# Kernel optimization log

Measured on AMD Instinct MI355X. Metric: run time of the kernel, lower is better.

The kernel has to match this reference:

```python
import jax, jax.numpy as jnp
import numpy as np

N_TOKENS = 262144
D_IN = 128
D_OUT = 128
N_EXPERTS = 8


def setup_inputs() -> dict:
    key = jax.random.key(0)
    k1, k2, k3, k4 = jax.random.split(key, 4)
    x = jax.random.normal(k1, (N_TOKENS, D_IN), dtype=jnp.float32)
    split = jax.random.randint(k2, (N_TOKENS,), 0, N_EXPERTS, dtype=jnp.int64)
    # Per-expert Linear params (one "model" per unique split value).
    W = jax.random.normal(k3, (N_EXPERTS, D_IN, D_OUT), dtype=jnp.float32) / np.sqrt(D_IN)
    b = jax.random.normal(k4, (N_EXPERTS, D_OUT), dtype=jnp.float32)
    return {"x": x, "split": split, "W": W, "b": b}


def reference(x, split, W, b):
    # Original 'alone' path: gather rows per unique split value, apply
    # model[split_value], concat, then reorder via argsort of the gathered
    # indices. That composition is exactly a per-token expert apply:
    #   out[t] = x[t] @ W[split[t]] + b[split[t]]
    # Computed densely per expert (fixed shapes, jit-friendly), then select.
    y_all = jnp.einsum('nf,efg->eng', x, W) + b[:, None, :]  # [E, N, d_out]
    tok = jnp.arange(x.shape[0])
    return y_all[split, tok]  # [N, d_out]
```

## Files before the change

kernel.cpp:

```cpp
#include <hip/hip_runtime.h>


typedef __bf16 bf16x8 __attribute__((ext_vector_type(8)));
typedef unsigned short u16x8 __attribute__((ext_vector_type(8)));
typedef float f32x4 __attribute__((ext_vector_type(4)));

__device__ __forceinline__ unsigned short f2bf(float f) {
    unsigned u = __builtin_bit_cast(unsigned, f);
    u += 0x7FFFu + ((u >> 16) & 1u);
    return (unsigned short)(u >> 16);
}
__device__ __forceinline__ unsigned pack2(float a, float b) {
    return (unsigned)f2bf(a) | ((unsigned)f2bf(b) << 16);
}

__global__ void k_wt(const float* __restrict__ W, unsigned short* __restrict__ Wt) {
    __shared__ float T[16][132];
    int e = blockIdx.x >> 3;
    int g0 = (blockIdx.x & 7) << 4;
    const float* We = W + e * 128 * 128;
    #pragma unroll
    for (int i = 0; i < 2; ++i) {
        int idx = i * 256 + threadIdx.x;
        int f = idx >> 2, q = idx & 3;
        float4 v = *(const float4*)(We + f * 128 + g0 + q * 4);
        T[q * 4 + 0][f] = v.x; T[q * 4 + 1][f] = v.y;
        T[q * 4 + 2][f] = v.z; T[q * 4 + 3][f] = v.w;
    }
    __syncthreads();
    int g = threadIdx.x >> 4, fc = threadIdx.x & 15;
    u16x8 o;
    #pragma unroll
    for (int j = 0; j < 8; ++j) o[j] = f2bf(T[g][fc * 8 + j]);
    *(u16x8*)(Wt + ((e * 128 + g0 + g) * 128 + fc * 8)) = o;
}

#define NT 256

__global__ __launch_bounds__(512) void k_fused(
    const float* __restrict__ x, const int* __restrict__ split,
    const float* __restrict__ bias, const unsigned short* __restrict__ Wt,
    float* __restrict__ out) {

    __shared__ unsigned short A[NT * 128];
    __shared__ int hcnt[8], startE[8];
    __shared__ int dest[NT], trow[NT];
    __shared__ int exT[24], rbT[24], limT[24];
    __shared__ int Tn;

    const int tid = threadIdx.x;
    const long t0 = (long)blockIdx.x * NT;

    if (tid < 8) hcnt[tid] = 0;
    __syncthreads();

    float4 xv[16];
    const float* xb = x + t0 * 128;
    #pragma unroll
    for (int rr = 0; rr < 16; ++rr)
        xv[rr] = *(const float4*)(xb + (rr * 512 + tid) * 4);

    int e = 0, rank = 0;
    if (tid < NT) {
        e = split[t0 + tid];
        rank = atomicAdd(&hcnt[e], 1);
    }
    __syncthreads();

    if (tid == 0) {
        int acc = 0, T = 0;
        for (int ee = 0; ee < 8; ++ee) {
            int c = hcnt[ee];
            startE[ee] = acc;
            for (int k = 0; k < c; k += 16) {
                exT[T] = ee; rbT[T] = acc + k;
                limT[T] = (c - k < 16) ? (c - k) : 16; T++;
            }
            acc += c;
        }
        Tn = T;
    }
    __syncthreads();

    if (tid < NT) {
        int s = startE[e] + rank;
        dest[tid] = s;
        trow[s] = tid;
    }
    __syncthreads();

    #pragma unroll
    for (int rr = 0; rr < 16; ++rr) {
        int c = rr * 512 + tid;
        int row = c >> 5;
        int s = dest[row];
        int fc = (c & 31) >> 1;
        int half = c & 1;
        unsigned d0 = pack2(xv[rr].x, xv[rr].y);
        unsigned d1 = pack2(xv[rr].z, xv[rr].w);
        unsigned short* p = A + s * 128 + ((fc ^ (s & 7)) << 3) + half * 4;
        *(uint2*)p = make_uint2(d0, d1);
    }
    __syncthreads();

    const int lane = tid & 63, w = tid >> 6;
    const int l15 = lane & 15, lq = lane >> 4;
    const int T = Tn;

    bf16x8 bfrag[4];
    float bv = 0.f;
    int preve = -1;

    for (int tau = 0; tau < T; ++tau) {
        int ee = exT[tau], rb = rbT[tau], lim = limT[tau];
        if (ee != preve) {
            preve = ee;
            const unsigned short* Wb = Wt + ee * 16384 + (w * 16 + l15) * 128;
            #pragma unroll
            for (int kk = 0; kk < 4; ++kk)
                bfrag[kk] = *(const bf16x8*)(Wb + (kk * 4 + lq) * 8);
            bv = bias[ee * 128 + w * 16 + l15];
        }
        int srow = rb + l15;
        srow = srow < NT - 1 ? srow : NT - 1;
        f32x4 acc = {0.f, 0.f, 0.f, 0.f};
        #pragma unroll
        for (int kk = 0; kk < 4; ++kk) {
            int fc = kk * 4 + lq;
            bf16x8 a = *(const bf16x8*)(A + srow * 128 + ((fc ^ (srow & 7)) << 3));
            acc = __builtin_amdgcn_mfma_f32_16x16x32_bf16(a, bfrag[kk], acc, 0, 0, 0);
        }
        #pragma unroll
        for (int r = 0; r < 4; ++r) {
            int ri = lq * 4 + r;
            if (ri < lim) {
                int tokl = trow[rb + ri];
                out[(t0 + tokl) * 128 + w * 16 + l15] = acc[r] + bv;
            }
        }
    }
}

extern "C" void kernel_launch(void* const* d_in, const int* in_sizes, int n_in,
                              void* d_out, int out_size, void* d_ws, size_t ws_size,
                              hipStream_t stream) {
    const float* x     = (const float*)d_in[0];
    const int*   split = (const int*)d_in[1];
    const float* W     = (const float*)d_in[2];
    const float* bias  = (const float*)d_in[3];
    float* out = (float*)d_out;

    int n = in_sizes[1];
    unsigned short* Wt = (unsigned short*)d_ws;

    k_wt<<<64, 256, 0, stream>>>(W, Wt);
    k_fused<<<n / NT, 512, 0, stream>>>(x, split, bias, Wt, out);
}
```

Measured before the change: 83.02 us.

## Halve block tokens, use 4 waves with two output tiles each, ballot-based expert ranking

```diff
diff --git a/kernel.cpp b/kernel.cpp
--- a/kernel.cpp
+++ b/kernel.cpp
@@ -35,55 +35,64 @@
     *(u16x8*)(Wt + ((e * 128 + g0 + g) * 128 + fc * 8)) = o;
 }
 
-#define NT 256
+#define NT 128
 
-__global__ __launch_bounds__(512) void k_fused(
+__global__ __launch_bounds__(256, 4) void k_fused(
     const float* __restrict__ x, const int* __restrict__ split,
     const float* __restrict__ bias, const unsigned short* __restrict__ Wt,
     float* __restrict__ out) {
 
     __shared__ unsigned short A[NT * 128];
-    __shared__ int hcnt[8], startE[8];
+    __shared__ int wcnt[16];
+    __shared__ int startE[8], off1[8];
     __shared__ int dest[NT], trow[NT];
-    __shared__ int exT[24], rbT[24], limT[24];
+    __shared__ int exT[16], rbT[16], limT[16];
     __shared__ int Tn;
 
     const int tid = threadIdx.x;
+    const int lane = tid & 63, w = tid >> 6;
     const long t0 = (long)blockIdx.x * NT;
-
-    if (tid < 8) hcnt[tid] = 0;
-    __syncthreads();
 
     float4 xv[16];
     const float* xb = x + t0 * 128;
     #pragma unroll
     for (int rr = 0; rr < 16; ++rr)
-        xv[rr] = *(const float4*)(xb + (rr * 512 + tid) * 4);
+        xv[rr] = *(const float4*)(xb + (rr * 256 + tid) * 4);
 
-    int e = 0, rank = 0;
-    if (tid < NT) {
-        e = split[t0 + tid];
-        rank = atomicAdd(&hcnt[e], 1);
+    int e = 255, myrank = 0;
+    if (tid < NT) e = split[t0 + tid];
+    const unsigned long long below = (lane == 63) ? ~0ull >> 1 : (1ull << lane) - 1;
+    #pragma unroll
+    for (int ee = 0; ee < 8; ++ee) {
+        unsigned long long m = __ballot(e == ee);
+        if (e == ee) myrank = (int)__popcll(m & below);
+        if (w < 2 && lane == ee) wcnt[w * 8 + ee] = (int)__popcll(m);
     }
     __syncthreads();
 
-    if (tid == 0) {
-        int acc = 0, T = 0;
-        for (int ee = 0; ee < 8; ++ee) {
-            int c = hcnt[ee];
-            startE[ee] = acc;
-            for (int k = 0; k < c; k += 16) {
-                exT[T] = ee; rbT[T] = acc + k;
-                limT[T] = (c - k < 16) ? (c - k) : 16; T++;
-            }
-            acc += c;
+    if (w == 0 && lane < 8) {
+        int c0 = wcnt[lane], c1 = wcnt[8 + lane];
+        int cE = c0 + c1;
+        int v = cE;
+        #pragma unroll
+        for (int d = 1; d < 8; d <<= 1) { int t2 = __shfl_up(v, d, 64); if (lane >= d) v += t2; }
+        int sE = v - cE;
+        startE[lane] = sE; off1[lane] = sE + c0;
+        int nt = (cE + 15) >> 4;
+        int u = nt;
+        #pragma unroll
+        for (int d = 1; d < 8; d <<= 1) { int t2 = __shfl_up(u, d, 64); if (lane >= d) u += t2; }
+        int tb = u - nt;
+        for (int k = 0; k < nt; ++k) {
+            exT[tb + k] = lane; rbT[tb + k] = sE + k * 16;
+            int rem = cE - k * 16; limT[tb + k] = rem < 16 ? rem : 16;
         }
-        Tn = T;
+        if (lane == 7) Tn = u;
     }
     __syncthreads();
 
     if (tid < NT) {
-        int s = startE[e] + rank;
+        int s = (w == 0 ? startE[e] : off1[e]) + myrank;
         dest[tid] = s;
         trow[s] = tid;
     }
@@ -91,51 +100,54 @@
 
     #pragma unroll
     for (int rr = 0; rr < 16; ++rr) {
-        int c = rr * 512 + tid;
+        int c = rr * 256 + tid;
         int row = c >> 5;
         int s = dest[row];
         int fc = (c & 31) >> 1;
         int half = c & 1;
         unsigned d0 = pack2(xv[rr].x, xv[rr].y);
         unsigned d1 = pack2(xv[rr].z, xv[rr].w);
-        unsigned short* p = A + s * 128 + ((fc ^ (s & 7)) << 3) + half * 4;
-        *(uint2*)p = make_uint2(d0, d1);
+        *(uint2*)(A + s * 128 + ((fc ^ (s & 7)) << 3) + half * 4) = make_uint2(d0, d1);
     }
     __syncthreads();
 
-    const int lane = tid & 63, w = tid >> 6;
     const int l15 = lane & 15, lq = lane >> 4;
     const int T = Tn;
 
-    bf16x8 bfrag[4];
-    float bv = 0.f;
+    bf16x8 bfrag[2][4];
+    float bv[2];
     int preve = -1;
 
     for (int tau = 0; tau < T; ++tau) {
         int ee = exT[tau], rb = rbT[tau], lim = limT[tau];
         if (ee != preve) {
             preve = ee;
-            const unsigned short* Wb = Wt + ee * 16384 + (w * 16 + l15) * 128;
             #pragma unroll
-            for (int kk = 0; kk < 4; ++kk)
-                bfrag[kk] = *(const bf16x8*)(Wb + (kk * 4 + lq) * 8);
-            bv = bias[ee * 128 + w * 16 + l15];
+            for (int j = 0; j < 2; ++j) {
+                const unsigned short* Wb = Wt + ee * 16384 + (w * 32 + j * 16 + l15) * 128;
+                #pragma unroll
+                for (int kk = 0; kk < 4; ++kk)
+                    bfrag[j][kk] = *(const bf16x8*)(Wb + (kk * 4 + lq) * 8);
+                bv[j] = bias[ee * 128 + w * 32 + j * 16 + l15];
+            }
         }
         int srow = rb + l15;
-        srow = srow < NT - 1 ? srow : NT - 1;
-        f32x4 acc = {0.f, 0.f, 0.f, 0.f};
+        srow = srow < NT ? srow : NT - 1;
+        f32x4 acc0 = {0.f, 0.f, 0.f, 0.f}, acc1 = {0.f, 0.f, 0.f, 0.f};
         #pragma unroll
         for (int kk = 0; kk < 4; ++kk) {
             int fc = kk * 4 + lq;
             bf16x8 a = *(const bf16x8*)(A + srow * 128 + ((fc ^ (srow & 7)) << 3));
-            acc = __builtin_amdgcn_mfma_f32_16x16x32_bf16(a, bfrag[kk], acc, 0, 0, 0);
+            acc0 = __builtin_amdgcn_mfma_f32_16x16x32_bf16(a, bfrag[0][kk], acc0, 0, 0, 0);
+            acc1 = __builtin_amdgcn_mfma_f32_16x16x32_bf16(a, bfrag[1][kk], acc1, 0, 0, 0);
         }
         #pragma unroll
         for (int r = 0; r < 4; ++r) {
             int ri = lq * 4 + r;
             if (ri < lim) {
-                int tokl = trow[rb + ri];
-                out[(t0 + tokl) * 128 + w * 16 + l15] = acc[r] + bv;
+                long o = (t0 + trow[rb + ri]) * 128 + w * 32 + l15;
+                out[o]      = acc0[r] + bv[0];
+                out[o + 16] = acc1[r] + bv[1];
             }
         }
     }
@@ -154,5 +166,5 @@
     unsigned short* Wt = (unsigned short*)d_ws;
 
     k_wt<<<64, 256, 0, stream>>>(W, Wt);
-    k_fused<<<n / NT, 512, 0, stream>>>(x, split, bias, Wt, out);
+    k_fused<<<n / NT, 256, 0, stream>>>(x, split, bias, Wt, out);
 }
```

Measured after the change: 95.67 us. 15.2% more time.

## Persistent double-buffered kernel with async LDS loads and register-resident expert weights

Applied to the files above, without the earlier changes.

```diff
diff --git a/kernel.cpp b/kernel.cpp
--- a/kernel.cpp
+++ b/kernel.cpp
@@ -5,13 +5,13 @@
 typedef unsigned short u16x8 __attribute__((ext_vector_type(8)));
 typedef float f32x4 __attribute__((ext_vector_type(4)));
 
+typedef const __attribute__((address_space(1))) void* gptr_t;
+typedef __attribute__((address_space(3))) void* lptr_t;
+
 __device__ __forceinline__ unsigned short f2bf(float f) {
     unsigned u = __builtin_bit_cast(unsigned, f);
     u += 0x7FFFu + ((u >> 16) & 1u);
     return (unsigned short)(u >> 16);
-}
-__device__ __forceinline__ unsigned pack2(float a, float b) {
-    return (unsigned)f2bf(a) | ((unsigned)f2bf(b) << 16);
 }
 
 __global__ void k_wt(const float* __restrict__ W, unsigned short* __restrict__ Wt) {
@@ -35,107 +35,117 @@
     *(u16x8*)(Wt + ((e * 128 + g0 + g) * 128 + fc * 8)) = o;
 }
 
-#define NT 256
+#define NTOK 64
+#define GRID 256
 
-__global__ __launch_bounds__(512) void k_fused(
+__global__ __launch_bounds__(512, 2) void k_fused(
     const float* __restrict__ x, const int* __restrict__ split,
     const float* __restrict__ bias, const unsigned short* __restrict__ Wt,
-    float* __restrict__ out) {
+    float* __restrict__ out, int iters) {
 
-    __shared__ unsigned short A[NT * 128];
-    __shared__ int hcnt[8], startE[8];
-    __shared__ int dest[NT], trow[NT];
-    __shared__ int exT[24], rbT[24], limT[24];
-    __shared__ int Tn;
+    __shared__ float buf[2][NTOK * 128];
+    __shared__ int sL[2][NTOK];
+    __shared__ int trowL[2][NTOK];
+    __shared__ int cntL[2][8], startL[2][8];
 
     const int tid = threadIdx.x;
-    const long t0 = (long)blockIdx.x * NT;
-
-    if (tid < 8) hcnt[tid] = 0;
-    __syncthreads();
-
-    float4 xv[16];
-    const float* xb = x + t0 * 128;
-    #pragma unroll
-    for (int rr = 0; rr < 16; ++rr)
-        xv[rr] = *(const float4*)(xb + (rr * 512 + tid) * 4);
-
-    int e = 0, rank = 0;
-    if (tid < NT) {
-        e = split[t0 + tid];
-        rank = atomicAdd(&hcnt[e], 1);
-    }
-    __syncthreads();
-
-    if (tid == 0) {
-        int acc = 0, T = 0;
-        for (int ee = 0; ee < 8; ++ee) {
-            int c = hcnt[ee];
-            startE[ee] = acc;
-            for (int k = 0; k < c; k += 16) {
-                exT[T] = ee; rbT[T] = acc + k;
-                limT[T] = (c - k < 16) ? (c - k) : 16; T++;
-            }
-            acc += c;
-        }
-        Tn = T;
-    }
-    __syncthreads();
-
-    if (tid < NT) {
-        int s = startE[e] + rank;
-        dest[tid] = s;
-        trow[s] = tid;
-    }
-    __syncthreads();
-
-    #pragma unroll
-    for (int rr = 0; rr < 16; ++rr) {
-        int c = rr * 512 + tid;
-        int row = c >> 5;
-        int s = dest[row];
-        int fc = (c & 31) >> 1;
-        int half = c & 1;
-        unsigned d0 = pack2(xv[rr].x, xv[rr].y);
-        unsigned d1 = pack2(xv[rr].z, xv[rr].w);
-        unsigned short* p = A + s * 128 + ((fc ^ (s & 7)) << 3) + half * 4;
-        *(uint2*)p = make_uint2(d0, d1);
-    }
-    __syncthreads();
-
     const int lane = tid & 63, w = tid >> 6;
     const int l15 = lane & 15, lq = lane >> 4;
-    const int T = Tn;
+    const int tbase = (int)blockIdx.x * iters;
 
-    bf16x8 bfrag[4];
-    float bv = 0.f;
-    int preve = -1;
+    bf16x8 bf_[8][4];
+    float bv_[8];
+    #pragma unroll
+    for (int ee = 0; ee < 8; ++ee) {
+        #pragma unroll
+        for (int kk = 0; kk < 4; ++kk)
+            bf_[ee][kk] = *(const bf16x8*)(Wt + ((ee * 128 + w * 16 + l15) * 128 + kk * 32 + lq * 8));
+        bv_[ee] = bias[ee * 128 + w * 16 + l15];
+    }
 
-    for (int tau = 0; tau < T; ++tau) {
-        int ee = exT[tau], rb = rbT[tau], lim = limT[tau];
-        if (ee != preve) {
-            preve = ee;
-            const unsigned short* Wb = Wt + ee * 16384 + (w * 16 + l15) * 128;
+    auto stage_x = [&](int tile, int p) {
+        const char* gb = (const char*)(x + (long)tile * NTOK * 128);
+        #pragma unroll
+        for (int i = 0; i < 4; ++i) {
+            int L = (w * 4 + i) * 64 + lane;
+            int row = L >> 5;
+            int c = (L & 31) ^ (row & 31);
+            __builtin_amdgcn_global_load_lds(
+                (gptr_t)(const void*)(gb + row * 512 + c * 16),
+                (lptr_t)(void*)((char*)&buf[p][0] + (w * 4 + i) * 1024),
+                16, 0, 0);
+        }
+    };
+    auto stage_split = [&](int tile, int p) {
+        __builtin_amdgcn_global_load_lds(
+            (gptr_t)(const void*)(split + tile * NTOK + lane),
+            (lptr_t)(void*)&sL[p][0], 4, 0, 0);
+    };
+    auto ballot_meta = [&](int p) {
+        int ev = sL[p][lane];
+        unsigned long long below = (1ull << lane) - 1;
+        int myrank = 0;
+        #pragma unroll
+        for (int ee = 0; ee < 8; ++ee) {
+            unsigned long long m = __ballot(ev == ee);
+            if (ev == ee) myrank = (int)__popcll(m & below);
+            if (lane == ee) cntL[p][lane] = (int)__popcll(m);
+        }
+        if (lane < 8) {
+            int s = 0;
             #pragma unroll
-            for (int kk = 0; kk < 4; ++kk)
-                bfrag[kk] = *(const bf16x8*)(Wb + (kk * 4 + lq) * 8);
-            bv = bias[ee * 128 + w * 16 + l15];
+            for (int j = 0; j < 8; ++j) s += (j < lane) ? cntL[p][j] : 0;
+            startL[p][lane] = s;
         }
-        int srow = rb + l15;
-        srow = srow < NT - 1 ? srow : NT - 1;
-        f32x4 acc = {0.f, 0.f, 0.f, 0.f};
+        trowL[p][startL[p][ev] + myrank] = lane;
+    };
+
+    if (w == 3) { stage_split(tbase, 0); stage_split(tbase + 1 < tbase + iters ? tbase + 1 : tbase, 1); }
+    stage_x(tbase, 0);
+    asm volatile("s_waitcnt vmcnt(0)" ::: "memory");
+    __builtin_amdgcn_s_barrier();
+    if (w == 0) ballot_meta(0);
+
+    for (int t = 0; t < iters; ++t) {
+        const int p = t & 1;
+        __builtin_amdgcn_s_barrier();
+        int t1 = (t + 1 < iters) ? t + 1 : iters - 1;
+        int t2 = (t + 2 < iters) ? t + 2 : iters - 1;
+        if (w == 3) stage_split(tbase + t2, p);
+        stage_x(tbase + t1, p ^ 1);
+        asm volatile("s_waitcnt vmcnt(5)" ::: "memory");
+        __builtin_amdgcn_s_barrier();
+        if (w == 0) ballot_meta(p ^ 1);
+
+        const long t0 = (long)(tbase + t) * NTOK;
         #pragma unroll
-        for (int kk = 0; kk < 4; ++kk) {
-            int fc = kk * 4 + lq;
-            bf16x8 a = *(const bf16x8*)(A + srow * 128 + ((fc ^ (srow & 7)) << 3));
-            acc = __builtin_amdgcn_mfma_f32_16x16x32_bf16(a, bfrag[kk], acc, 0, 0, 0);
-        }
-        #pragma unroll
-        for (int r = 0; r < 4; ++r) {
-            int ri = lq * 4 + r;
-            if (ri < lim) {
-                int tokl = trow[rb + ri];
-                out[(t0 + tokl) * 128 + w * 16 + l15] = acc[r] + bv;
+        for (int ee = 0; ee < 8; ++ee) {
+            int cnt = cntL[p][ee];
+            int st = startL[p][ee];
+            for (int k2 = 0; k2 * 16 < cnt; ++k2) {
+                int rb = st + k2 * 16;
+                int rem = cnt - k2 * 16;
+                int lim = rem < 16 ? rem : 16;
+                int sr = rb + l15; sr = sr < NTOK ? sr : NTOK - 1;
+                int srow = trowL[p][sr];
+                f32x4 acc = {0.f, 0.f, 0.f, 0.f};
+                #pragma unroll
+                for (int kk = 0; kk < 4; ++kk) {
+                    int c0 = kk * 8 + lq * 2;
+                    float4 va = *(const float4*)&buf[p][srow * 128 + ((c0 ^ (srow & 31)) << 2)];
+                    float4 vb = *(const float4*)&buf[p][srow * 128 + (((c0 + 1) ^ (srow & 31)) << 2)];
+                    u16x8 u;
+                    u[0] = f2bf(va.x); u[1] = f2bf(va.y); u[2] = f2bf(va.z); u[3] = f2bf(va.w);
+                    u[4] = f2bf(vb.x); u[5] = f2bf(vb.y); u[6] = f2bf(vb.z); u[7] = f2bf(vb.w);
+                    acc = __builtin_amdgcn_mfma_f32_16x16x32_bf16(
+                        __builtin_bit_cast(bf16x8, u), bf_[ee][kk], acc, 0, 0, 0);
+                }
+                #pragma unroll
+                for (int r = 0; r < 4; ++r) {
+                    int ri = lq * 4 + r;
+                    if (ri < lim)
+                        out[(t0 + trowL[p][rb + ri]) * 128 + w * 16 + l15] = acc[r] + bv_[ee];
+                }
             }
         }
     }
@@ -153,6 +163,9 @@
     int n = in_sizes[1];
     unsigned short* Wt = (unsigned short*)d_ws;
 
+    int ntiles = n / NTOK;
+    int iters = ntiles / GRID;
+
     k_wt<<<64, 256, 0, stream>>>(W, Wt);
-    k_fused<<<n / NT, 512, 0, stream>>>(x, split, bias, Wt, out);
+    k_fused<<<GRID, 512, 0, stream>>>(x, split, bias, Wt, out, iters);
 }
```

After: 137.6 us. 1.66x slower.

## Replace block-level LDS token sort with wave-level ballot sort and direct global loads

Applied to the files above, without the earlier changes.

```diff
diff --git a/kernel.cpp b/kernel.cpp
--- a/kernel.cpp
+++ b/kernel.cpp
@@ -9,9 +9,6 @@
     unsigned u = __builtin_bit_cast(unsigned, f);
     u += 0x7FFFu + ((u >> 16) & 1u);
     return (unsigned short)(u >> 16);
-}
-__device__ __forceinline__ unsigned pack2(float a, float b) {
-    return (unsigned)f2bf(a) | ((unsigned)f2bf(b) << 16);
 }
 
 __global__ void k_wt(const float* __restrict__ W, unsigned short* __restrict__ Wt) {
@@ -35,107 +32,80 @@
     *(u16x8*)(Wt + ((e * 128 + g0 + g) * 128 + fc * 8)) = o;
 }
 
-#define NT 256
+#define WTOK 64
 
-__global__ __launch_bounds__(512) void k_fused(
+__global__ __launch_bounds__(256) void k_moe(
     const float* __restrict__ x, const int* __restrict__ split,
     const float* __restrict__ bias, const unsigned short* __restrict__ Wt,
     float* __restrict__ out) {
 
-    __shared__ unsigned short A[NT * 128];
-    __shared__ int hcnt[8], startE[8];
-    __shared__ int dest[NT], trow[NT];
-    __shared__ int exT[24], rbT[24], limT[24];
-    __shared__ int Tn;
+    const int tid = threadIdx.x;
+    const int lane = tid & 63;
+    const int w = tid >> 6;
+    const int l15 = lane & 15, lq = lane >> 4;
+    const int col0 = w * 32;
+    const long t0 = (long)blockIdx.x * WTOK;
+    const float* xw = x + t0 * 128;
 
-    const int tid = threadIdx.x;
-    const long t0 = (long)blockIdx.x * NT;
-
-    if (tid < 8) hcnt[tid] = 0;
-    __syncthreads();
-
-    float4 xv[16];
-    const float* xb = x + t0 * 128;
+    int ev = split[t0 + lane];
+    const unsigned long long below = (1ull << lane) - 1;
+    int rank = 0;
+    int cnt[8], start[8];
+    int run = 0;
     #pragma unroll
-    for (int rr = 0; rr < 16; ++rr)
-        xv[rr] = *(const float4*)(xb + (rr * 512 + tid) * 4);
-
-    int e = 0, rank = 0;
-    if (tid < NT) {
-        e = split[t0 + tid];
-        rank = atomicAdd(&hcnt[e], 1);
+    for (int ee = 0; ee < 8; ++ee) {
+        unsigned long long m = __ballot(ev == ee);
+        if (ev == ee) rank = (int)__popcll(m & below);
+        cnt[ee] = (int)__popcll(m);
+        start[ee] = run; run += cnt[ee];
     }
-    __syncthreads();
-
-    if (tid == 0) {
-        int acc = 0, T = 0;
-        for (int ee = 0; ee < 8; ++ee) {
-            int c = hcnt[ee];
-            startE[ee] = acc;
-            for (int k = 0; k < c; k += 16) {
-                exT[T] = ee; rbT[T] = acc + k;
-                limT[T] = (c - k < 16) ? (c - k) : 16; T++;
-            }
-            acc += c;
-        }
-        Tn = T;
-    }
-    __syncthreads();
-
-    if (tid < NT) {
-        int s = startE[e] + rank;
-        dest[tid] = s;
-        trow[s] = tid;
-    }
-    __syncthreads();
+    int slot = start[ev] + rank;
+    int tokslot = __builtin_amdgcn_ds_permute(slot << 2, lane);
 
     #pragma unroll
-    for (int rr = 0; rr < 16; ++rr) {
-        int c = rr * 512 + tid;
-        int row = c >> 5;
-        int s = dest[row];
-        int fc = (c & 31) >> 1;
-        int half = c & 1;
-        unsigned d0 = pack2(xv[rr].x, xv[rr].y);
-        unsigned d1 = pack2(xv[rr].z, xv[rr].w);
-        unsigned short* p = A + s * 128 + ((fc ^ (s & 7)) << 3) + half * 4;
-        *(uint2*)p = make_uint2(d0, d1);
-    }
-    __syncthreads();
+    for (int ee = 0; ee < 8; ++ee) {
+        int c = cnt[ee];
+        if (c == 0) continue;
 
-    const int lane = tid & 63, w = tid >> 6;
-    const int l15 = lane & 15, lq = lane >> 4;
-    const int T = Tn;
-
-    bf16x8 bfrag[4];
-    float bv = 0.f;
-    int preve = -1;
-
-    for (int tau = 0; tau < T; ++tau) {
-        int ee = exT[tau], rb = rbT[tau], lim = limT[tau];
-        if (ee != preve) {
-            preve = ee;
-            const unsigned short* Wb = Wt + ee * 16384 + (w * 16 + l15) * 128;
-            #pragma unroll
-            for (int kk = 0; kk < 4; ++kk)
-                bfrag[kk] = *(const bf16x8*)(Wb + (kk * 4 + lq) * 8);
-            bv = bias[ee * 128 + w * 16 + l15];
-        }
-        int srow = rb + l15;
-        srow = srow < NT - 1 ? srow : NT - 1;
-        f32x4 acc = {0.f, 0.f, 0.f, 0.f};
+        bf16x8 bfr0[4], bfr1[4];
         #pragma unroll
         for (int kk = 0; kk < 4; ++kk) {
-            int fc = kk * 4 + lq;
-            bf16x8 a = *(const bf16x8*)(A + srow * 128 + ((fc ^ (srow & 7)) << 3));
-            acc = __builtin_amdgcn_mfma_f32_16x16x32_bf16(a, bfrag[kk], acc, 0, 0, 0);
+            bfr0[kk] = *(const bf16x8*)(Wt + (ee * 128 + col0 + l15) * 128 + kk * 32 + lq * 8);
+            bfr1[kk] = *(const bf16x8*)(Wt + (ee * 128 + col0 + 16 + l15) * 128 + kk * 32 + lq * 8);
         }
-        #pragma unroll
-        for (int r = 0; r < 4; ++r) {
-            int ri = lq * 4 + r;
-            if (ri < lim) {
-                int tokl = trow[rb + ri];
-                out[(t0 + tokl) * 128 + w * 16 + l15] = acc[r] + bv;
+        float bv0 = bias[ee * 128 + col0 + l15];
+        float bv1 = bias[ee * 128 + col0 + 16 + l15];
+
+        int sE = start[ee];
+        for (int rb = sE; rb < sE + c; rb += 16) {
+            int lim = sE + c - rb; lim = lim < 16 ? lim : 16;
+
+            int idx = rb + l15; idx = idx > 63 ? 63 : idx;
+            int rowA = __builtin_amdgcn_ds_bpermute(idx << 2, tokslot);
+
+            const float* xr = xw + rowA * 128 + lq * 8;
+            f32x4 acc0 = {0.f, 0.f, 0.f, 0.f}, acc1 = {0.f, 0.f, 0.f, 0.f};
+            #pragma unroll
+            for (int kk = 0; kk < 4; ++kk) {
+                float4 lo = *(const float4*)(xr + kk * 32);
+                float4 hi = *(const float4*)(xr + kk * 32 + 4);
+                u16x8 u;
+                u[0] = f2bf(lo.x); u[1] = f2bf(lo.y); u[2] = f2bf(lo.z); u[3] = f2bf(lo.w);
+                u[4] = f2bf(hi.x); u[5] = f2bf(hi.y); u[6] = f2bf(hi.z); u[7] = f2bf(hi.w);
+                bf16x8 a = __builtin_bit_cast(bf16x8, u);
+                acc0 = __builtin_amdgcn_mfma_f32_16x16x32_bf16(a, bfr0[kk], acc0, 0, 0, 0);
+                acc1 = __builtin_amdgcn_mfma_f32_16x16x32_bf16(a, bfr1[kk], acc1, 0, 0, 0);
+            }
+
+            #pragma unroll
+            for (int r = 0; r < 4; ++r) {
+                int ss = rb + lq * 4 + r; ss = ss > 63 ? 63 : ss;
+                int rowS = __builtin_amdgcn_ds_bpermute(ss << 2, tokslot);
+                if (lq * 4 + r < lim) {
+                    float* o = out + (t0 + rowS) * 128 + col0 + l15;
+                    o[0]  = acc0[r] + bv0;
+                    o[16] = acc1[r] + bv1;
+                }
             }
         }
     }
@@ -154,5 +124,5 @@
     unsigned short* Wt = (unsigned short*)d_ws;
 
     k_wt<<<64, 256, 0, stream>>>(W, Wt);
-    k_fused<<<n / NT, 512, 0, stream>>>(x, split, bias, Wt, out);
+    k_moe<<<n / WTOK, 256, 0, stream>>>(x, split, bias, Wt, out);
 }
```

Measured after the change: 238.1 us. 187% more time.
